# Kernel optimization log

Hardware: AMD Instinct MI355X
Metric: run time of the kernel (lower is better)

## Reference

```python
import jax, jax.numpy as jnp
import numpy as np

B, C, OUT, HD = 2, 256, 256, 32
H = C // HD                      # num_heads = 8
SCALE = HD ** -0.5
N = 40962                        # icosahedron level-6 vertices
N_TOP, TOP = 2562, 16
N_DOWN, DOWN = 2562, 19
M = N_TOP * TOP + N_DOWN * DOWN  # flattened window positions (pad row = index M)
MLP_HID = int(OUT * 2.0)
BN_EPS = 1e-5


def _build_geometry(seed=0):
    rng = np.random.default_rng(seed)
    # every vertex appears at least once; extras create overlapping patches
    flat = np.concatenate([rng.permutation(N), rng.integers(0, N, M - N)]).astype(np.int64)
    top = flat[:N_TOP * TOP].reshape(N_TOP, TOP)
    down = flat[N_TOP * TOP:].reshape(N_DOWN, DOWN)
    counts = np.bincount(flat, minlength=N)
    K = int(counts.max())
    order = np.argsort(flat, kind='stable')
    v_sorted = flat[order]
    cum = np.concatenate([[0], np.cumsum(counts)])
    pos = np.arange(M) - cum[v_sorted]          # within-group rank
    reverse = np.full((N, K), M, dtype=np.int64)  # pad -> zero row
    reverse[v_sorted, pos] = order
    cnt_inv = (1.0 / counts).astype(np.float32)
    return top, down, reverse, cnt_inv


def setup_inputs() -> dict:
    key = jax.random.key(0)
    ks = jax.random.split(key, 8)
    top, down, reverse, cnt_inv = _build_geometry(0)
    s_in, s_out, s_hid = C ** -0.5, OUT ** -0.5, MLP_HID ** -0.5
    return {
        'x': jax.random.normal(ks[0], (B, C, N), jnp.float32),
        'Wqkv': jax.random.normal(ks[1], (C, 3 * C), jnp.float32) * s_in,
        'bqkv': jnp.zeros((3 * C,), jnp.float32),
        'Wproj': jax.random.normal(ks[2], (C, OUT), jnp.float32) * s_in,
        'bproj': jnp.zeros((OUT,), jnp.float32),
        'Wres': jax.random.normal(ks[3], (C, OUT), jnp.float32) * s_in,
        'bres': jnp.zeros((OUT,), jnp.float32),
        'Wm1': jax.random.normal(ks[4], (OUT, MLP_HID), jnp.float32) * s_out,
        'bm1': jnp.zeros((MLP_HID,), jnp.float32),
        'Wm2': jax.random.normal(ks[5], (MLP_HID, OUT), jnp.float32) * s_hid,
        'bm2': jnp.zeros((OUT,), jnp.float32),
        'gamma': jnp.ones((OUT,), jnp.float32),
        'beta': jnp.zeros((OUT,), jnp.float32),
        'cnt_inv': jnp.asarray(cnt_inv),
        'top_idx': jnp.asarray(top),
        'down_idx': jnp.asarray(down),
        'reverse_idx': jnp.asarray(reverse),
    }


def reference(x, Wqkv, bqkv, Wproj, bproj, Wres, bres, Wm1, bm1, Wm2, bm2,
              gamma, beta, cnt_inv, top_idx, down_idx, reverse_idx):
    xt = jnp.transpose(x, (0, 2, 1))                      # B,N,C
    res = xt @ Wres + bres                                # B,N,OUT
    qkv = (xt @ Wqkv + bqkv).reshape(B, N, 3, H, HD)
    qkv = jnp.transpose(qkv, (2, 0, 3, 1, 4))             # 3,B,H,N,hd
    q, k, v = qkv[0] * SCALE, qkv[1], qkv[2]

    def win_attn(idx):
        qw, kw, vw = q[:, :, idx], k[:, :, idx], v[:, :, idx]   # B,H,nw,w,hd
        a = jax.nn.softmax(jnp.einsum('bhnjc,bhnkc->bhnjk', qw, kw), axis=-1)
        return jnp.einsum('bhnjk,bhnkc->bhnjc', a, vw)

    x_top = win_attn(top_idx).reshape(B, H, N_TOP * TOP, HD)
    x_down = win_attn(down_idx).reshape(B, H, N_DOWN * DOWN, HD)
    xw = jnp.concatenate([x_top, x_down], axis=2)         # B,H,M,hd
    xw = jnp.concatenate([xw, jnp.zeros((B, H, 1, HD), xw.dtype)], axis=2)  # pad row
    xg = xw[:, :, reverse_idx, :]                         # B,H,N,K,hd
    xa = (xg * cnt_inv[None, None, :, None, None]).sum(axis=3)  # B,H,N,hd
    xf = jnp.transpose(xa, (0, 2, 1, 3)).reshape(B, N, C)

    out = xf @ Wproj + bproj + res                        # B,N,OUT
    res2 = (out @ Wm1 + bm1) @ Wm2 + bm2                  # no activation (faithful)

    out_t = jnp.transpose(out, (0, 2, 1))                 # B,OUT,N
    r2t = jnp.transpose(res2, (0, 2, 1))
    mean = r2t.mean(axis=(0, 2), keepdims=True)
    var = r2t.var(axis=(0, 2), keepdims=True)             # biased, batch stats
    bn = (r2t - mean) * jax.lax.rsqrt(var + BN_EPS)
    bn = bn * gamma[None, :, None] + beta[None, :, None]
    return out_t + bn
```

## Files before the change

kernel.cpp:

```cpp
#include <hip/hip_runtime.h>
#include <stdint.h>

typedef unsigned short u16;
typedef __bf16 bf16x8 __attribute__((ext_vector_type(8)));
typedef float f32x4 __attribute__((ext_vector_type(4)));

#define B_    2
#define C_    256
#define N_    40962
#define BN_   (B_ * N_)
#define H_    8
#define HD_   32
#define NTOP  2562
#define TOPW  16
#define NDOWN 2562
#define DOWNW 19
#define M_    (NTOP*TOPW + NDOWN*DOWNW)
#define SCALE_ 0.17677669529663687f
#define BN_EPS 1e-5f

__device__ __forceinline__ float b2f(u16 u) {
    union { uint32_t i; float f; } v; v.i = ((uint32_t)u) << 16; return v.f;
}
__device__ __forceinline__ u16 f2b(float f) {
    union { float f; uint32_t i; } v; v.f = f;
    uint32_t r = v.i + 0x7fffu + ((v.i >> 16) & 1u);
    return (u16)(r >> 16);
}
__device__ __forceinline__ float ld(const void* p, size_t i, int isf32) {
    return isf32 ? ((const float*)p)[i] : b2f(((const u16*)p)[i]);
}

__global__ void probe_k(const void* __restrict__ x, int* __restrict__ flag) {
    int lane = threadIdx.x;
    u16 v = ((const u16*)x)[2 * lane];
    int e = (v >> 7) & 0xff;
    bool ok = (e >= 118 && e <= 134);
    unsigned long long m = __ballot(ok);
    if (lane == 0) *flag = (__popcll(m) < 32) ? 1 : 0;
}

__global__ void wcat_k(const void* __restrict__ Wqkv, const void* __restrict__ Wres,
                       const void* __restrict__ Wproj,
                       u16* __restrict__ WcatT, u16* __restrict__ WprojT,
                       const int* __restrict__ flag) {
    const int f = *flag;
    int k = blockIdx.x, t = threadIdx.x;
    for (int j = t; j < 768; j += 256) WcatT[(size_t)j * 256 + k] = f2b(ld(Wqkv, (size_t)k * 768 + j, f));
    WcatT[(size_t)(768 + t) * 256 + k] = f2b(ld(Wres, (size_t)k * 256 + t, f));
    WprojT[(size_t)t * 256 + k] = f2b(ld(Wproj, (size_t)k * 256 + t, f));
}

__global__ void biasprep_k(const void* bqkv, const void* bres, const void* bproj,
                           float* bias_cat, float* bias_proj, const int* __restrict__ flag) {
    const int f = *flag;
    int g = blockIdx.x * 256 + threadIdx.x;
    if (g < 768) bias_cat[g] = ld(bqkv, g, f);
    else if (g < 1024) bias_cat[g] = ld(bres, g - 768, f);
    else if (g < 1280) bias_proj[g - 1024] = ld(bproj, g - 1024, f);
}

__global__ __launch_bounds__(256) void wf_k(const void* __restrict__ Wm1, const void* __restrict__ Wm2,
                                            u16* __restrict__ WfT, const int* __restrict__ flag) {
    const int f = *flag;
    __shared__ float row[512];
    int i = blockIdx.x, t = threadIdx.x;
    row[t] = ld(Wm1, (size_t)i * 512 + t, f);
    row[t + 256] = ld(Wm1, (size_t)i * 512 + 256 + t, f);
    __syncthreads();
    float acc = 0.f;
    for (int k = 0; k < 512; ++k) acc += row[k] * ld(Wm2, (size_t)k * 256 + t, f);
    WfT[(size_t)t * 256 + i] = f2b(acc);
}

__global__ void bf_k(const void* bm1, const void* __restrict__ Wm2, const void* bm2,
                     float* bf, const int* __restrict__ flag) {
    const int f = *flag;
    int t = threadIdx.x;
    float acc = ld(bm2, t, f);
    for (int k = 0; k < 512; ++k) acc += ld(bm1, k, f) * ld(Wm2, (size_t)k * 256 + t, f);
    bf[t] = acc;
}

__global__ __launch_bounds__(256) void gemm_qkv_k(
    const void* __restrict__ x, const u16* __restrict__ WcatT,
    const float* __restrict__ bias, u16* __restrict__ Out, const int* __restrict__ flag)
{
    const int isf32 = *flag;
    __shared__ __align__(16) u16 As[64][264];
    __shared__ __align__(16) u16 Bs[64][264];
    const int tid = threadIdx.x;
    const int R0 = blockIdx.x * 64;
    const int wave = tid >> 6, lane = tid & 63;
    const int quad = lane >> 4, mrow = lane & 15;

    {
        const int n = tid & 63;
        const int kg = tid >> 6;
        const int g = R0 + n;
        const bool valid = (g < BN_);
        const int b = (g >= N_) ? 1 : 0;
        const int nn = g - b * N_;
#pragma unroll
        for (int j = 0; j < 8; ++j) {
            const int k0 = kg * 8 + j * 32;
            u16 tmp[8];
            if (valid) {
                if (isf32) {
                    const float* xp = (const float*)x + (size_t)(b * 256 + k0) * N_ + nn;
#pragma unroll
                    for (int i = 0; i < 8; ++i) tmp[i] = f2b(xp[(size_t)i * N_]);
                } else {
                    const u16* xp = (const u16*)x + (size_t)(b * 256 + k0) * N_ + nn;
#pragma unroll
                    for (int i = 0; i < 8; ++i) tmp[i] = xp[(size_t)i * N_];
                }
            } else {
#pragma unroll
                for (int i = 0; i < 8; ++i) tmp[i] = 0;
            }
            *reinterpret_cast<uint4*>(&As[n][k0]) = *reinterpret_cast<const uint4*>(tmp);
        }
    }

    for (int ct = 0; ct < 16; ++ct) {
        const int C0 = ct * 64;
        __syncthreads();
#pragma unroll
        for (int it = 0; it < 8; ++it) {
            int e = it * 256 + tid;
            int col = e >> 5, ks = (e & 31) * 8;
            uint4 v = *reinterpret_cast<const uint4*>(WcatT + (size_t)(C0 + col) * 256 + ks);
            *reinterpret_cast<uint4*>(&Bs[col][ks]) = v;
        }
        __syncthreads();
        f32x4 acc[4] = {f32x4{0,0,0,0}, f32x4{0,0,0,0}, f32x4{0,0,0,0}, f32x4{0,0,0,0}};
#pragma unroll
        for (int kc = 0; kc < 8; ++kc) {
            bf16x8 bfrag = *reinterpret_cast<const bf16x8*>(&Bs[wave * 16 + mrow][kc * 32 + quad * 8]);
#pragma unroll
            for (int t2 = 0; t2 < 4; ++t2) {
                bf16x8 afrag = *reinterpret_cast<const bf16x8*>(&As[t2 * 16 + mrow][kc * 32 + quad * 8]);
                acc[t2] = __builtin_amdgcn_mfma_f32_16x16x32_bf16(afrag, bfrag, acc[t2], 0, 0, 0);
            }
        }
        const int col = C0 + wave * 16 + mrow;
        const float bcol = bias[col];
#pragma unroll
        for (int t2 = 0; t2 < 4; ++t2) {
#pragma unroll
            for (int r = 0; r < 4; ++r) {
                int row = R0 + t2 * 16 + quad * 4 + r;
                if (row < BN_) {
                    Out[(size_t)row * 1024 + col] = f2b(acc[t2][r] + bcol);
                }
            }
        }
    }
}

template<bool ADD_RES, bool OUT_F32>
__global__ __launch_bounds__(256) void gemm_k(
    const u16* __restrict__ A, int ldA, const u16* __restrict__ Bt,
    const float* __restrict__ bias,
    const u16* __restrict__ resp, int ldRes,
    void* __restrict__ Out, int ldOut, int Rtot)
{
    __shared__ __align__(16) u16 As[64][264];
    __shared__ __align__(16) u16 Bs[64][264];
    const int tid = threadIdx.x;
    const int R0 = blockIdx.x * 64;
    const int wave = tid >> 6, lane = tid & 63;
    const int quad = lane >> 4, mrow = lane & 15;

#pragma unroll
    for (int it = 0; it < 8; ++it) {
        int e = it * 256 + tid;
        int row = e >> 5, ks = (e & 31) * 8;
        uint4 v = make_uint4(0u, 0u, 0u, 0u);
        if (R0 + row < Rtot)
            v = *reinterpret_cast<const uint4*>(A + (size_t)(R0 + row) * ldA + ks);
        *reinterpret_cast<uint4*>(&As[row][ks]) = v;
    }

    for (int ct = 0; ct < 4; ++ct) {
        const int C0 = ct * 64;
        __syncthreads();
#pragma unroll
        for (int it = 0; it < 8; ++it) {
            int e = it * 256 + tid;
            int col = e >> 5, ks = (e & 31) * 8;
            uint4 v = *reinterpret_cast<const uint4*>(Bt + (size_t)(C0 + col) * 256 + ks);
            *reinterpret_cast<uint4*>(&Bs[col][ks]) = v;
        }
        __syncthreads();
        f32x4 acc[4] = {f32x4{0,0,0,0}, f32x4{0,0,0,0}, f32x4{0,0,0,0}, f32x4{0,0,0,0}};
#pragma unroll
        for (int kc = 0; kc < 8; ++kc) {
            bf16x8 bfrag = *reinterpret_cast<const bf16x8*>(&Bs[wave * 16 + mrow][kc * 32 + quad * 8]);
#pragma unroll
            for (int t2 = 0; t2 < 4; ++t2) {
                bf16x8 afrag = *reinterpret_cast<const bf16x8*>(&As[t2 * 16 + mrow][kc * 32 + quad * 8]);
                acc[t2] = __builtin_amdgcn_mfma_f32_16x16x32_bf16(afrag, bfrag, acc[t2], 0, 0, 0);
            }
        }
        const int col = C0 + wave * 16 + mrow;
        const float bcol = bias[col];
#pragma unroll
        for (int t2 = 0; t2 < 4; ++t2) {
#pragma unroll
            for (int r = 0; r < 4; ++r) {
                int row = R0 + t2 * 16 + quad * 4 + r;
                if (row < Rtot) {
                    float v = acc[t2][r] + bcol;
                    if (ADD_RES) v += b2f(resp[(size_t)row * ldRes + col]);
                    if (OUT_F32) ((float*)Out)[(size_t)row * ldOut + col] = v;
                    else         ((u16*)Out)[(size_t)row * ldOut + col] = f2b(v);
                }
            }
        }
    }
}

template<int W>
__global__ __launch_bounds__(256) void attn_k(const u16* __restrict__ qkv, const int* __restrict__ widx,
                                              u16* __restrict__ xw, int mbase)
{
    const int w = blockIdx.x, b = blockIdx.y;
    const int tid = threadIdx.x;
    __shared__ int wi[W];
    __shared__ __align__(16) float Ks[W][H_][36];
    __shared__ __align__(16) float Vs[W][H_][36];
    if (tid < W) wi[tid] = widx[w * W + tid];
    __syncthreads();
    for (int e = tid; e < W * 32; e += 256) {
        int j = e >> 5, seg = e & 31;
        size_t base = ((size_t)(b * N_ + wi[j])) * 1024 + 256 + seg * 8;
        uint4 kv = *reinterpret_cast<const uint4*>(qkv + base);
        uint4 vv = *reinterpret_cast<const uint4*>(qkv + base + 256);
        int h = seg >> 2, c0 = (seg & 3) * 8;
        const u16* kp = (const u16*)&kv; const u16* vp = (const u16*)&vv;
#pragma unroll
        for (int t = 0; t < 8; ++t) {
            Ks[j][h][c0 + t] = b2f(kp[t]);
            Vs[j][h][c0 + t] = b2f(vp[t]);
        }
    }
    __syncthreads();

    if (tid < W * H_) {
        const int j = tid >> 3, h = tid & 7;
        float qr[32];
        {
            size_t qb = ((size_t)(b * N_ + wi[j])) * 1024 + h * 32;
#pragma unroll
            for (int s4 = 0; s4 < 4; ++s4) {
                uint4 qv = *reinterpret_cast<const uint4*>(qkv + qb + s4 * 8);
                const u16* qp = (const u16*)&qv;
#pragma unroll
                for (int t = 0; t < 8; ++t) qr[s4 * 8 + t] = b2f(qp[t]) * SCALE_;
            }
        }
        float p[W];
        float mx = -1e30f;
#pragma unroll
        for (int jj = 0; jj < W; ++jj) {
            const float* kr = &Ks[jj][h][0];
            float s = 0.f;
#pragma unroll
            for (int c = 0; c < 32; ++c) s += qr[c] * kr[c];
            p[jj] = s;
            mx = fmaxf(mx, s);
        }
        float sum = 0.f;
#pragma unroll
        for (int jj = 0; jj < W; ++jj) { p[jj] = __expf(p[jj] - mx); sum += p[jj]; }
        const float inv = 1.0f / sum;
        float o[32];
#pragma unroll
        for (int c = 0; c < 32; ++c) o[c] = 0.f;
#pragma unroll
        for (int jj = 0; jj < W; ++jj) {
            const float pj = p[jj];
            const float* vr = &Vs[jj][h][0];
#pragma unroll
            for (int c = 0; c < 32; ++c) o[c] += pj * vr[c];
        }
        const int m = mbase + w * W + j;
        size_t off = ((size_t)b * (M_ + 1) + m) * 256 + h * 32;
#pragma unroll
        for (int s4 = 0; s4 < 4; ++s4) {
            uint32_t w0 = (uint32_t)f2b(o[s4 * 8 + 0] * inv) | ((uint32_t)f2b(o[s4 * 8 + 1] * inv) << 16);
            uint32_t w1 = (uint32_t)f2b(o[s4 * 8 + 2] * inv) | ((uint32_t)f2b(o[s4 * 8 + 3] * inv) << 16);
            uint32_t w2 = (uint32_t)f2b(o[s4 * 8 + 4] * inv) | ((uint32_t)f2b(o[s4 * 8 + 5] * inv) << 16);
            uint32_t w3 = (uint32_t)f2b(o[s4 * 8 + 6] * inv) | ((uint32_t)f2b(o[s4 * 8 + 7] * inv) << 16);
            *reinterpret_cast<uint4*>(xw + off + s4 * 8) = make_uint4(w0, w1, w2, w3);
        }
    }
}

__global__ __launch_bounds__(256) void gather_k(const u16* __restrict__ xw, const int* __restrict__ rev,
                                                const void* __restrict__ cnt_inv, u16* __restrict__ xfp,
                                                int K, const int* __restrict__ flag)
{
    const int f = *flag;
    int gid = blockIdx.x * 4 + (threadIdx.x >> 6);
    if (gid >= BN_) return;
    int b = (gid >= N_) ? 1 : 0;
    int n = gid - b * N_;
    int c4 = (threadIdx.x & 63) * 4;
    float a0 = 0, a1 = 0, a2 = 0, a3 = 0;
    const int* rp = rev + (size_t)n * K;
    for (int k = 0; k < K; ++k) {
        int idx = rp[k];
        if (idx < M_) {
            ushort4 v = *reinterpret_cast<const ushort4*>(xw + ((size_t)b * (M_ + 1) + idx) * 256 + c4);
            a0 += b2f(v.x); a1 += b2f(v.y); a2 += b2f(v.z); a3 += b2f(v.w);
        }
    }
    float ci = ld(cnt_inv, n, f);
    ushort4 o;
    o.x = f2b(a0 * ci); o.y = f2b(a1 * ci); o.z = f2b(a2 * ci); o.w = f2b(a3 * ci);
    *reinterpret_cast<ushort4*>(xfp + (size_t)gid * 1024 + c4) = o;
}

#define STATS_BLOCKS 512
__global__ __launch_bounds__(256) void stats_k(const float* __restrict__ res2, float* __restrict__ sums) {
    const int tid = threadIdx.x;
    const int c4 = (tid & 63) * 4;
    const int rsub = tid >> 6;
    float s[4] = {0.f, 0.f, 0.f, 0.f};
    float q[4] = {0.f, 0.f, 0.f, 0.f};
    for (int r = blockIdx.x * 4 + rsub; r < BN_; r += STATS_BLOCKS * 4) {
        float4 v = *reinterpret_cast<const float4*>(res2 + (size_t)r * 256 + c4);
        s[0] += v.x; q[0] += v.x * v.x;
        s[1] += v.y; q[1] += v.y * v.y;
        s[2] += v.z; q[2] += v.z * v.z;
        s[3] += v.w; q[3] += v.w * v.w;
    }
    __shared__ float rs[256][4];
    __shared__ float rq[256][4];
#pragma unroll
    for (int j = 0; j < 4; ++j) { rs[tid][j] = s[j]; rq[tid][j] = q[j]; }
    __syncthreads();
    if (tid < 64) {
#pragma unroll
        for (int j = 0; j < 4; ++j) {
            float a = rs[tid][j] + rs[tid + 64][j] + rs[tid + 128][j] + rs[tid + 192][j];
            float b = rq[tid][j] + rq[tid + 64][j] + rq[tid + 128][j] + rq[tid + 192][j];
            atomicAdd(&sums[c4 + j], a);
            atomicAdd(&sums[256 + c4 + j], b);
        }
    }
}

__global__ void bnfin_k(const float* sums, const void* gamma, const void* beta, float* ss,
                        const int* __restrict__ flag) {
    const int f = *flag;
    int c = threadIdx.x;
    float mean = sums[c] * (1.0f / BN_);
    float var = sums[256 + c] * (1.0f / BN_) - mean * mean;
    float inv = rsqrtf(fmaxf(var, 0.f) + BN_EPS);
    float sc = ld(gamma, c, f) * inv;
    ss[c] = sc;
    ss[256 + c] = ld(beta, c, f) - mean * sc;
}

__global__ __launch_bounds__(256) void final_k(const u16* __restrict__ outb, const float* __restrict__ res2,
                                               const float* __restrict__ ss, void* __restrict__ y,
                                               const int* __restrict__ flag)
{
    const int isf32 = *flag;
    __shared__ __align__(16) float tile[64][65];
    const int n0 = blockIdx.x * 64, o0 = blockIdx.y * 64, b = blockIdx.z;
    const int tid = threadIdx.x;
    {
        const int ln = tid >> 2, os = (tid & 3) * 16;
        int n = n0 + ln;
        if (n < N_) {
            size_t base = ((size_t)(b * N_ + n)) * 256 + o0 + os;
            uint4 ov0 = *reinterpret_cast<const uint4*>(outb + base);
            uint4 ov1 = *reinterpret_cast<const uint4*>(outb + base + 8);
            const u16* op = (const u16*)&ov0;
            const u16* op1 = (const u16*)&ov1;
            float4 rv[4];
#pragma unroll
            for (int q = 0; q < 4; ++q) rv[q] = *reinterpret_cast<const float4*>(res2 + base + q * 4);
            const float* rp = (const float*)&rv[0];
#pragma unroll
            for (int j = 0; j < 16; ++j) {
                int oc = o0 + os + j;
                float ob = (j < 8) ? b2f(op[j]) : b2f(op1[j - 8]);
                tile[ln][os + j] = ob + rp[j] * ss[oc] + ss[256 + oc];
            }
        }
    }
    __syncthreads();
    {
        const int wave = tid >> 6, lane = tid & 63;
        int n = n0 + lane;
        if (n < N_) {
            if (isf32) {
                float* yp = (float*)y;
#pragma unroll
                for (int r0 = 0; r0 < 64; r0 += 4) {
                    int r = r0 + wave;
                    int oc = o0 + r;
                    yp[((size_t)(b * 256 + oc)) * N_ + n] = tile[lane][r];
                }
            } else {
                u16* yp = (u16*)y;
#pragma unroll
                for (int r0 = 0; r0 < 64; r0 += 4) {
                    int r = r0 + wave;
                    int oc = o0 + r;
                    yp[((size_t)(b * 256 + oc)) * N_ + n] = f2b(tile[lane][r]);
                }
            }
        }
    }
}

static const size_t OFF_QKV   = 0;
static const size_t OFF_XW    = 167780352;
static const size_t OFF_SMALL = 259603456;

extern "C" void kernel_launch(void* const* d_in, const int* in_sizes, int n_in,
                              void* d_out, int out_size, void* d_ws, size_t ws_size,
                              hipStream_t stream) {
    const void* x     = d_in[0];
    const void* Wqkv  = d_in[1];
    const void* bqkv  = d_in[2];
    const void* Wproj = d_in[3];
    const void* bproj = d_in[4];
    const void* Wres  = d_in[5];
    const void* bres  = d_in[6];
    const void* Wm1   = d_in[7];
    const void* bm1   = d_in[8];
    const void* Wm2   = d_in[9];
    const void* bm2   = d_in[10];
    const void* gamma = d_in[11];
    const void* beta  = d_in[12];
    const void* cnt_inv = d_in[13];
    const int* top_idx = (const int*)d_in[14];
    const int* down_idx = (const int*)d_in[15];
    const int* rev   = (const int*)d_in[16];
    const int K = in_sizes[16] / N_;

    char* ws = (char*)d_ws;
    u16*  qkvres  = (u16*)(ws + OFF_QKV);
    float* res2   = (float*)(ws + OFF_QKV);
    u16*  xw      = (u16*)(ws + OFF_XW);
    u16*  outb    = (u16*)(ws + OFF_XW);
    u16*  WcatT   = (u16*)(ws + OFF_SMALL);
    u16*  WfT     = (u16*)(ws + OFF_SMALL + 524288);
    float* bias_cat  = (float*)(ws + OFF_SMALL + 655360);
    float* bias_proj = (float*)(ws + OFF_SMALL + 659456);
    float* bfv       = (float*)(ws + OFF_SMALL + 663552);
    float* stats     = (float*)(ws + OFF_SMALL + 667648);
    float* ssbuf     = (float*)(ws + OFF_SMALL + 671744);
    int*   flag      = (int*)(ws + OFF_SMALL + 675840);
    u16*  WprojT     = (u16*)(ws + OFF_SMALL + 679936);

    probe_k<<<1, 64, 0, stream>>>(x, flag);

    wcat_k<<<256, 256, 0, stream>>>(Wqkv, Wres, Wproj, WcatT, WprojT, flag);
    biasprep_k<<<5, 256, 0, stream>>>(bqkv, bres, bproj, bias_cat, bias_proj, flag);
    wf_k<<<256, 256, 0, stream>>>(Wm1, Wm2, WfT, flag);
    bf_k<<<1, 256, 0, stream>>>(bm1, Wm2, bm2, bfv, flag);

    gemm_qkv_k<<<1281, 256, 0, stream>>>(x, WcatT, bias_cat, qkvres, flag);

    attn_k<TOPW><<<dim3(NTOP, B_), 256, 0, stream>>>(qkvres, top_idx, xw, 0);
    attn_k<DOWNW><<<dim3(NDOWN, B_), 256, 0, stream>>>(qkvres, down_idx, xw, NTOP * TOPW);

    gather_k<<<(BN_ + 3) / 4, 256, 0, stream>>>(xw, rev, cnt_inv, qkvres, K, flag);

    gemm_k<true, false><<<1281, 256, 0, stream>>>(
        qkvres, 1024, WprojT, bias_proj, qkvres + 768, 1024, (void*)outb, 256, BN_);

    gemm_k<false, true><<<1281, 256, 0, stream>>>(
        outb, 256, WfT, bfv, nullptr, 0, (void*)res2, 256, BN_);

    (void)hipMemsetAsync(stats, 0, 512 * sizeof(float), stream);
    stats_k<<<STATS_BLOCKS, 256, 0, stream>>>(res2, stats);
    bnfin_k<<<1, 256, 0, stream>>>(stats, gamma, beta, ssbuf, flag);

    final_k<<<dim3(641, 4, 2), 256, 0, stream>>>(outb, res2, ssbuf, d_out, flag);
}
```

Baseline: 904.7 us.

## Coalesce x loads in QKV GEMM, hold A in registers, XCD-swizzle blocks

The QKV GEMM gets a fast path for full tiles where each thread loads one channel's 64 contiguous positions, instead of strided per-channel loads. The generic GEMM now keeps the A tile in registers as MFMA fragments instead of shared memory, dropping LDS traffic and space. Both kernels remap block indices so neighbouring tiles land on the same XCD, aiming for better L2 locality. Holding 32 uint4 of A per thread raises register pressure, and the transposed LDS stores in the fast path may cause bank conflicts.

```diff
diff --git a/kernel.cpp b/kernel.cpp
--- a/kernel.cpp
+++ b/kernel.cpp
@@ -31,6 +31,12 @@
     return isf32 ? ((const float*)p)[i] : b2f(((const u16*)p)[i]);
 }
 
+__device__ __forceinline__ int xcd_swz_1281(int bx) {
+    const int q = 160, r = 1;
+    int xcd = bx & 7, o = bx >> 3;
+    return (xcd < r ? xcd * (q + 1) : r * (q + 1) + (xcd - r) * q) + o;
+}
+
 __global__ void probe_k(const void* __restrict__ x, int* __restrict__ flag) {
     int lane = threadIdx.x;
     u16 v = ((const u16*)x)[2 * lane];
@@ -90,11 +96,34 @@
     __shared__ __align__(16) u16 As[64][264];
     __shared__ __align__(16) u16 Bs[64][264];
     const int tid = threadIdx.x;
-    const int R0 = blockIdx.x * 64;
+    const int bx = xcd_swz_1281(blockIdx.x);
+    const int R0 = bx * 64;
     const int wave = tid >> 6, lane = tid & 63;
     const int quad = lane >> 4, mrow = lane & 15;
 
-    {
+    const bool fastA = (R0 + 64 <= N_) || (R0 >= N_ && R0 + 64 <= BN_);
+    if (fastA) {
+        const int b = (R0 >= N_) ? 1 : 0;
+        const int nn = R0 - b * N_;
+        const int k = tid;
+        if (isf32) {
+            const float* xp = (const float*)x + (size_t)(b * 256 + k) * N_ + nn;
+#pragma unroll
+            for (int j = 0; j < 32; ++j) {
+                float2 v = *reinterpret_cast<const float2*>(xp + 2 * j);
+                As[2 * j][k] = f2b(v.x);
+                As[2 * j + 1][k] = f2b(v.y);
+            }
+        } else {
+            const u16* xp = (const u16*)x + (size_t)(b * 256 + k) * N_ + nn;
+#pragma unroll
+            for (int j = 0; j < 32; ++j) {
+                uint32_t v = *reinterpret_cast<const uint32_t*>(xp + 2 * j);
+                As[2 * j][k] = (u16)v;
+                As[2 * j + 1][k] = (u16)(v >> 16);
+            }
+        }
+    } else {
         const int n = tid & 63;
         const int kg = tid >> 6;
         const int g = R0 + n;
@@ -106,15 +135,8 @@
             const int k0 = kg * 8 + j * 32;
             u16 tmp[8];
             if (valid) {
-                if (isf32) {
-                    const float* xp = (const float*)x + (size_t)(b * 256 + k0) * N_ + nn;
-#pragma unroll
-                    for (int i = 0; i < 8; ++i) tmp[i] = f2b(xp[(size_t)i * N_]);
-                } else {
-                    const u16* xp = (const u16*)x + (size_t)(b * 256 + k0) * N_ + nn;
-#pragma unroll
-                    for (int i = 0; i < 8; ++i) tmp[i] = xp[(size_t)i * N_];
-                }
+#pragma unroll
+                for (int i = 0; i < 8; ++i) tmp[i] = f2b(ld(x, (size_t)(b * 256 + k0 + i) * N_ + nn, isf32));
             } else {
 #pragma unroll
                 for (int i = 0; i < 8; ++i) tmp[i] = 0;
@@ -166,21 +188,23 @@
     const u16* __restrict__ resp, int ldRes,
     void* __restrict__ Out, int ldOut, int Rtot)
 {
-    __shared__ __align__(16) u16 As[64][264];
     __shared__ __align__(16) u16 Bs[64][264];
     const int tid = threadIdx.x;
-    const int R0 = blockIdx.x * 64;
+    const int bx = xcd_swz_1281(blockIdx.x);
+    const int R0 = bx * 64;
     const int wave = tid >> 6, lane = tid & 63;
     const int quad = lane >> 4, mrow = lane & 15;
 
-#pragma unroll
-    for (int it = 0; it < 8; ++it) {
-        int e = it * 256 + tid;
-        int row = e >> 5, ks = (e & 31) * 8;
-        uint4 v = make_uint4(0u, 0u, 0u, 0u);
-        if (R0 + row < Rtot)
-            v = *reinterpret_cast<const uint4*>(A + (size_t)(R0 + row) * ldA + ks);
-        *reinterpret_cast<uint4*>(&As[row][ks]) = v;
+    uint4 afr[4][8];
+#pragma unroll
+    for (int t2 = 0; t2 < 4; ++t2) {
+        const int row = R0 + t2 * 16 + mrow;
+        const u16* ap = A + (size_t)row * ldA + quad * 8;
+#pragma unroll
+        for (int kc = 0; kc < 8; ++kc) {
+            afr[t2][kc] = (row < Rtot) ? *reinterpret_cast<const uint4*>(ap + kc * 32)
+                                       : make_uint4(0u, 0u, 0u, 0u);
+        }
     }
 
     for (int ct = 0; ct < 4; ++ct) {
@@ -200,7 +224,7 @@
             bf16x8 bfrag = *reinterpret_cast<const bf16x8*>(&Bs[wave * 16 + mrow][kc * 32 + quad * 8]);
 #pragma unroll
             for (int t2 = 0; t2 < 4; ++t2) {
-                bf16x8 afrag = *reinterpret_cast<const bf16x8*>(&As[t2 * 16 + mrow][kc * 32 + quad * 8]);
+                bf16x8 afrag = *reinterpret_cast<const bf16x8*>(&afr[t2][kc]);
                 acc[t2] = __builtin_amdgcn_mfma_f32_16x16x32_bf16(afrag, bfrag, acc[t2], 0, 0, 0);
             }
         }
```

After: 920.9 us. About the same (+1.8%).
